# Optimization experiments

Measured on AMD Instinct MI355X. Metric: run time of the kernel, lower is better.

The kernel has to match this reference:

```python
import jax, jax.numpy as jnp
import numpy as np

ALPHA = 1.0
BETA = 10.0
MARGIN = 0.5


def setup_inputs() -> dict:
    key = jax.random.key(0)
    k1, k2 = jax.random.split(key)
    emb = jax.random.normal(k1, (4096, 512), dtype=jnp.float32)
    # module docstring: embeddings are L2-normalized
    emb = emb / jnp.linalg.norm(emb, axis=1, keepdims=True)
    labels = jax.random.randint(k2, (4096,), 0, 64, dtype=jnp.int64)
    return {"embeddings": emb, "labels": labels}


def reference(embeddings, labels):
    n = embeddings.shape[0]
    sim = embeddings @ embeddings.T  # [n, n]
    labels_eq = labels[None, :] == labels[:, None]
    eye = jnp.eye(n, dtype=bool)
    pos_mask = labels_eq & ~eye
    neg_mask = ~labels_eq & ~eye

    # masked exp-sums (masked entries contribute 0, matching torch's
    # clone/NEG_INF/zero-out dance without materializing extra copies)
    pos_exp = jnp.where(pos_mask, jnp.exp(-ALPHA * (sim - MARGIN)), 0.0)
    neg_exp = jnp.where(neg_mask, jnp.exp(BETA * (sim - MARGIN)), 0.0)
    pos_term = (1.0 / ALPHA) * jnp.log1p(pos_exp.sum(axis=1))
    neg_term = (1.0 / BETA) * jnp.log1p(neg_exp.sum(axis=1))

    valid = pos_mask.any(axis=1) & neg_mask.any(axis=1)
    n_valid = valid.sum()
    total = jnp.where(valid, pos_term + neg_term, 0.0).sum()
    return jnp.where(n_valid > 0, total / jnp.maximum(n_valid, 1).astype(sim.dtype), 0.0)
```

## Files before the change

kernel.cpp:

```cpp
#include <hip/hip_runtime.h>
#include <hip/hip_bf16.h>

#define N 4096
#define D 512
#define MARGIN 0.5f
#define BETA 10.0f

typedef __attribute__((ext_vector_type(8))) short short8;
typedef __attribute__((ext_vector_type(4))) float floatx4;

__device__ inline unsigned short f2bf(float f) {
    unsigned u = __float_as_uint(f);
    u += 0x7fffu + ((u >> 16) & 1u);
    return (unsigned short)(u >> 16);
}

__global__ __launch_bounds__(256) void convert_bf16_kernel(
        const float4* __restrict__ in, ushort4* __restrict__ out,
        float* __restrict__ sums ) {
    int idx = blockIdx.x * 256 + threadIdx.x;
    if (idx < 2 * N) sums[idx] = 0.f;
    float4 v = in[idx];
    ushort4 o;
    o.x = f2bf(v.x); o.y = f2bf(v.y); o.z = f2bf(v.z); o.w = f2bf(v.w);
    out[idx] = o;
}

__global__ __launch_bounds__(256, 4) void ms_loss_gemm(
        const unsigned short* __restrict__ Ebf,
        const int* __restrict__ labels,
        float* __restrict__ pos_sum,
        float* __restrict__ neg_sum) {
    __shared__ unsigned short Atile[128 * 32];
    __shared__ unsigned short Btile[128 * 32];
    __shared__ int rlab[128];
    __shared__ int clab[128];

    int t = blockIdx.x;
    int bi = 0;
    while (t >= (32 - bi)) { t -= (32 - bi); ++bi; }
    const int bj = bi + t;
    const bool diag = (bi == bj);

    const int tid  = threadIdx.x;
    const int wave = tid >> 6;
    const int lane = tid & 63;
    const int quad = lane >> 4;
    const int lcol = lane & 15;
    const int wrow = wave >> 1;
    const int wcol = wave & 1;
    const int ibase = bi * 128;
    const int jbase = bj * 128;

    if (tid < 128)       rlab[tid]       = labels[ibase + tid];
    else                 clab[tid - 128] = labels[jbase + tid - 128];

    floatx4 acc[4][4];
#pragma unroll
    for (int mt = 0; mt < 4; ++mt)
#pragma unroll
        for (int nt = 0; nt < 4; ++nt)
            acc[mt][nt] = (floatx4){0.f, 0.f, 0.f, 0.f};

    const char* Eb = (const char*)Ebf;
    char* Ab = (char*)Atile;
    char* Bb = (char*)Btile;
    const char* Bread = diag ? Ab : Bb;
    const int srow = lane >> 2;
    const int sckb = ((lane & 3) ^ ((lane >> 3) & 3)) * 16;
    const int rdsw = ((lcol >> 1) & 3);

    for (int kt = 0; kt < D / 32; ++kt) {
        __syncthreads();
        const int kb = kt * 64;
#pragma unroll
        for (int it = 0; it < 2; ++it) {
            int r    = wave * 16 + it * 64 + srow;
            int ldso = wave * 1024 + it * 4096 + lane * 16;
            const char* ga = Eb + (size_t)(ibase + r) * (D * 2) + kb + sckb;
            __builtin_amdgcn_global_load_lds(
                (const __attribute__((address_space(1))) void*)ga,
                (__attribute__((address_space(3))) void*)(Ab + ldso), 16, 0, 0);
            if (!diag) {
                const char* gb = Eb + (size_t)(jbase + r) * (D * 2) + kb + sckb;
                __builtin_amdgcn_global_load_lds(
                    (const __attribute__((address_space(1))) void*)gb,
                    (__attribute__((address_space(3))) void*)(Bb + ldso), 16, 0, 0);
            }
        }
        __syncthreads();

        short8 a[4], b[4];
        const int rchunk = (quad ^ rdsw) * 16;
#pragma unroll
        for (int mt = 0; mt < 4; ++mt) {
            int r = wrow * 64 + mt * 16 + lcol;
            a[mt] = *(const short8*)(Ab + r * 64 + rchunk);
        }
#pragma unroll
        for (int nt = 0; nt < 4; ++nt) {
            int c = wcol * 64 + nt * 16 + lcol;
            b[nt] = *(const short8*)(Bread + c * 64 + rchunk);
        }
#pragma unroll
        for (int mt = 0; mt < 4; ++mt)
#pragma unroll
            for (int nt = 0; nt < 4; ++nt)
                acc[mt][nt] = __builtin_amdgcn_mfma_f32_16x16x32_bf16(
                    a[mt], b[nt], acc[mt][nt], 0, 0, 0);
    }

    int ljv[4], gjv[4];
#pragma unroll
    for (int nt = 0; nt < 4; ++nt) {
        int cl = wcol * 64 + nt * 16 + lcol;
        ljv[nt] = clab[cl];
        gjv[nt] = jbase + cl;
    }

    float colp[4] = {0.f, 0.f, 0.f, 0.f};
    float coln[4] = {0.f, 0.f, 0.f, 0.f};

#pragma unroll
    for (int mt = 0; mt < 4; ++mt) {
#pragma unroll
        for (int reg = 0; reg < 4; ++reg) {
            int rl = wrow * 64 + mt * 16 + quad * 4 + reg;
            int gi = ibase + rl;
            int li = rlab[rl];
            float p = 0.f, ng = 0.f;
#pragma unroll
            for (int nt = 0; nt < 4; ++nt) {
                float s = acc[mt][nt][reg];
                if (gi != gjv[nt]) {
                    if (li == ljv[nt]) {
                        float e = __expf(MARGIN - s);
                        p += e;  colp[nt] += e;
                    } else {
                        float e = __expf(BETA * (s - MARGIN));
                        ng += e; coln[nt] += e;
                    }
                }
            }
            p  += __shfl_xor(p, 1);   ng += __shfl_xor(ng, 1);
            p  += __shfl_xor(p, 2);   ng += __shfl_xor(ng, 2);
            p  += __shfl_xor(p, 4);   ng += __shfl_xor(ng, 4);
            p  += __shfl_xor(p, 8);   ng += __shfl_xor(ng, 8);
            if (lcol == 0) {
                atomicAdd(&pos_sum[gi], p);
                atomicAdd(&neg_sum[gi], ng);
            }
        }
    }

    if (!diag) {
#pragma unroll
        for (int nt = 0; nt < 4; ++nt) {
            float cp = colp[nt], cn = coln[nt];
            cp += __shfl_xor(cp, 16);  cn += __shfl_xor(cn, 16);
            cp += __shfl_xor(cp, 32);  cn += __shfl_xor(cn, 32);
            if (quad == 0) {
                int gj = gjv[nt];
                atomicAdd(&pos_sum[gj], cp);
                atomicAdd(&neg_sum[gj], cn);
            }
        }
    }
}

__global__ __launch_bounds__(256) void finalize_kernel(
        const float4* __restrict__ pos4, const float4* __restrict__ neg4,
        float* __restrict__ out) {
    __shared__ float sb[256];
    __shared__ int   sc[256];
    const int tid = threadIdx.x;
    float tot = 0.f;
    int cnt = 0;
#pragma unroll
    for (int it = 0; it < N / 4 / 256; ++it) {
        int i = it * 256 + tid;
        float4 p = pos4[i];
        float4 ng = neg4[i];
        const float* pp = (const float*)&p;
        const float* nn = (const float*)&ng;
#pragma unroll
        for (int j = 0; j < 4; ++j) {
            if (pp[j] > 0.f && nn[j] > 0.f) {
                tot += log1pf(pp[j]) + (1.0f / BETA) * log1pf(nn[j]);
                cnt += 1;
            }
        }
    }
    sb[tid] = tot; sc[tid] = cnt;
    __syncthreads();
    for (int s = 128; s > 0; s >>= 1) {
        if (tid < s) { sb[tid] += sb[tid + s]; sc[tid] += sc[tid + s]; }
        __syncthreads();
    }
    if (tid == 0) out[0] = (sc[0] > 0) ? sb[0] / (float)sc[0] : 0.f;
}

extern "C" void kernel_launch(void* const* d_in, const int* in_sizes, int n_in,
                              void* d_out, int out_size, void* d_ws, size_t ws_size,
                              hipStream_t stream) {
    const float* emb   = (const float*)d_in[0];
    const int* labels  = (const int*)d_in[1];
    float* out         = (float*)d_out;

    char* ws = (char*)d_ws;
    unsigned short* Ebf = (unsigned short*)ws;
    float* pos_sum = (float*)(ws + (size_t)N * D * 2);
    float* neg_sum = pos_sum + N;

    convert_bf16_kernel<<<(N * D / 4) / 256, 256, 0, stream>>>(
        (const float4*)emb, (ushort4*)Ebf, pos_sum);

    ms_loss_gemm<<<(32 * 33) / 2, 256, 0, stream>>>(Ebf, labels, pos_sum, neg_sum);

    finalize_kernel<<<1, 256, 0, stream>>>(
        (const float4*)pos_sum, (const float4*)neg_sum, out);
}
```

Before: 93.49 us.

## Double-buffer LDS tiles in GEMM and use wave-shuffle reduction in finalize

The GEMM loop now uses two LDS buffers per operand. The next k-tile is issued with global_load_lds while MFMAs run on the current one, so each iteration has one barrier instead of two. The finalize kernel runs 1024 threads, one float4 each, and reduces with warp shuffles instead of a shared-memory tree. Double buffering doubles LDS use per block, which may limit occupancy under the launch bound of 4 blocks per CU. The load-to-LDS completion also relies on the single barrier per iteration for correctness.

```diff
diff --git a/kernel.cpp b/kernel.cpp
--- a/kernel.cpp
+++ b/kernel.cpp
@@ -31,8 +31,8 @@
         const int* __restrict__ labels,
         float* __restrict__ pos_sum,
         float* __restrict__ neg_sum) {
-    __shared__ unsigned short Atile[128 * 32];
-    __shared__ unsigned short Btile[128 * 32];
+    __shared__ unsigned short Atile[2][128 * 32];
+    __shared__ unsigned short Btile[2][128 * 32];
     __shared__ int rlab[128];
     __shared__ int clab[128];
 
@@ -65,42 +65,52 @@
     const char* Eb = (const char*)Ebf;
     char* Ab = (char*)Atile;
     char* Bb = (char*)Btile;
-    const char* Bread = diag ? Ab : Bb;
     const int srow = lane >> 2;
     const int sckb = ((lane & 3) ^ ((lane >> 3) & 3)) * 16;
     const int rdsw = ((lcol >> 1) & 3);
 
+#define STAGE(BUF, KT)                                                         \
+    do {                                                                       \
+        const int kb_ = (KT) * 64;                                             \
+        _Pragma("unroll")                                                      \
+        for (int it_ = 0; it_ < 2; ++it_) {                                    \
+            int r_    = wave * 16 + it_ * 64 + srow;                           \
+            int ldso_ = (BUF) * 8192 + wave * 1024 + it_ * 4096 + lane * 16;   \
+            const char* ga_ = Eb + (size_t)(ibase + r_) * (D * 2) + kb_ + sckb;\
+            __builtin_amdgcn_global_load_lds(                                  \
+                (const __attribute__((address_space(1))) void*)ga_,            \
+                (__attribute__((address_space(3))) void*)(Ab + ldso_), 16, 0, 0);\
+            if (!diag) {                                                       \
+                const char* gb_ = Eb + (size_t)(jbase + r_) * (D * 2) + kb_ + sckb;\
+                __builtin_amdgcn_global_load_lds(                              \
+                    (const __attribute__((address_space(1))) void*)gb_,        \
+                    (__attribute__((address_space(3))) void*)(Bb + ldso_), 16, 0, 0);\
+            }                                                                  \
+        }                                                                      \
+    } while (0)
+
+    STAGE(0, 0);
+    __syncthreads();
+
+#pragma unroll 2
     for (int kt = 0; kt < D / 32; ++kt) {
-        __syncthreads();
-        const int kb = kt * 64;
-#pragma unroll
-        for (int it = 0; it < 2; ++it) {
-            int r    = wave * 16 + it * 64 + srow;
-            int ldso = wave * 1024 + it * 4096 + lane * 16;
-            const char* ga = Eb + (size_t)(ibase + r) * (D * 2) + kb + sckb;
-            __builtin_amdgcn_global_load_lds(
-                (const __attribute__((address_space(1))) void*)ga,
-                (__attribute__((address_space(3))) void*)(Ab + ldso), 16, 0, 0);
-            if (!diag) {
-                const char* gb = Eb + (size_t)(jbase + r) * (D * 2) + kb + sckb;
-                __builtin_amdgcn_global_load_lds(
-                    (const __attribute__((address_space(1))) void*)gb,
-                    (__attribute__((address_space(3))) void*)(Bb + ldso), 16, 0, 0);
-            }
-        }
-        __syncthreads();
+        const int cur = kt & 1;
+        if (kt < D / 32 - 1) STAGE(cur ^ 1, kt + 1);
+
+        const char* Ar = Ab + cur * 8192;
+        const char* Br = diag ? Ar : (Bb + cur * 8192);
 
         short8 a[4], b[4];
         const int rchunk = (quad ^ rdsw) * 16;
 #pragma unroll
         for (int mt = 0; mt < 4; ++mt) {
             int r = wrow * 64 + mt * 16 + lcol;
-            a[mt] = *(const short8*)(Ab + r * 64 + rchunk);
+            a[mt] = *(const short8*)(Ar + r * 64 + rchunk);
         }
 #pragma unroll
         for (int nt = 0; nt < 4; ++nt) {
             int c = wcol * 64 + nt * 16 + lcol;
-            b[nt] = *(const short8*)(Bread + c * 64 + rchunk);
+            b[nt] = *(const short8*)(Br + c * 64 + rchunk);
         }
 #pragma unroll
         for (int mt = 0; mt < 4; ++mt)
@@ -108,7 +118,10 @@
             for (int nt = 0; nt < 4; ++nt)
                 acc[mt][nt] = __builtin_amdgcn_mfma_f32_16x16x32_bf16(
                     a[mt], b[nt], acc[mt][nt], 0, 0, 0);
-    }
+
+        __syncthreads();
+    }
+#undef STAGE
 
     int ljv[4], gjv[4];
 #pragma unroll
@@ -168,36 +181,42 @@
     }
 }
 
-__global__ __launch_bounds__(256) void finalize_kernel(
+__global__ __launch_bounds__(1024) void finalize_kernel(
         const float4* __restrict__ pos4, const float4* __restrict__ neg4,
         float* __restrict__ out) {
-    __shared__ float sb[256];
-    __shared__ int   sc[256];
+    __shared__ float sb[16];
+    __shared__ int   sc[16];
     const int tid = threadIdx.x;
+    float4 p  = pos4[tid];
+    float4 ng = neg4[tid];
+    const float* pp = (const float*)&p;
+    const float* nn = (const float*)&ng;
     float tot = 0.f;
     int cnt = 0;
 #pragma unroll
-    for (int it = 0; it < N / 4 / 256; ++it) {
-        int i = it * 256 + tid;
-        float4 p = pos4[i];
-        float4 ng = neg4[i];
-        const float* pp = (const float*)&p;
-        const float* nn = (const float*)&ng;
-#pragma unroll
-        for (int j = 0; j < 4; ++j) {
-            if (pp[j] > 0.f && nn[j] > 0.f) {
-                tot += log1pf(pp[j]) + (1.0f / BETA) * log1pf(nn[j]);
-                cnt += 1;
-            }
-        }
-    }
-    sb[tid] = tot; sc[tid] = cnt;
+    for (int j = 0; j < 4; ++j) {
+        if (pp[j] > 0.f && nn[j] > 0.f) {
+            tot += log1pf(pp[j]) + (1.0f / BETA) * log1pf(nn[j]);
+            cnt += 1;
+        }
+    }
+#pragma unroll
+    for (int s = 1; s < 64; s <<= 1) {
+        tot += __shfl_xor(tot, s);
+        cnt += __shfl_xor(cnt, s);
+    }
+    if ((tid & 63) == 0) { sb[tid >> 6] = tot; sc[tid >> 6] = cnt; }
     __syncthreads();
-    for (int s = 128; s > 0; s >>= 1) {
-        if (tid < s) { sb[tid] += sb[tid + s]; sc[tid] += sc[tid + s]; }
-        __syncthreads();
-    }
-    if (tid == 0) out[0] = (sc[0] > 0) ? sb[0] / (float)sc[0] : 0.f;
+    if (tid < 16) {
+        float t2 = sb[tid];
+        int   c2 = sc[tid];
+#pragma unroll
+        for (int s = 1; s < 16; s <<= 1) {
+            t2 += __shfl_xor(t2, s);
+            c2 += __shfl_xor(c2, s);
+        }
+        if (tid == 0) out[0] = (c2 > 0) ? t2 / (float)c2 : 0.f;
+    }
 }
 
 extern "C" void kernel_launch(void* const* d_in, const int* in_sizes, int n_in,
@@ -217,6 +236,6 @@
 
     ms_loss_gemm<<<(32 * 33) / 2, 256, 0, stream>>>(Ebf, labels, pos_sum, neg_sum);
 
-    finalize_kernel<<<1, 256, 0, stream>>>(
+    finalize_kernel<<<1, 1024, 0, stream>>>(
         (const float4*)pos_sum, (const float4*)neg_sum, out);
 }
```

Result: faster. 88.85 us (-5.0%).
